# Kernel tuning notes

Hardware: AMD Instinct MI355X
Metric: run time of the kernel (lower is better)

Reference implementation:

```python
import jax, jax.numpy as jnp
import numpy as np

N_EMBD = 768
N_HEAD = 12
DIM_HEAD = N_EMBD // N_HEAD


def setup_inputs() -> dict:
    key = jax.random.key(0)
    k1, k2, k3 = jax.random.split(key, 3)
    B, T = 4, 2048
    x = jax.random.normal(k1, (B, T, N_EMBD), dtype=jnp.float32)
    # torch Linear(n_embd, 3*n_embd, bias=False): y = x @ W.T, W:[3C,C].
    # Store pre-transposed [C,3C] for direct matmul.
    s = 1.0 / np.sqrt(N_EMBD)
    W_qkv = jax.random.uniform(k2, (N_EMBD, 3 * N_EMBD), dtype=jnp.float32, minval=-s, maxval=s)
    W_proj = jax.random.uniform(k3, (N_EMBD, N_EMBD), dtype=jnp.float32, minval=-s, maxval=s)
    return {"x": x, "W_qkv": W_qkv, "W_proj": W_proj}


def reference(x, W_qkv, W_proj):
    B, T, C = x.shape
    qkv = x @ W_qkv                                  # [B,T,3C]
    q, k, v = jnp.split(qkv, 3, axis=-1)
    def heads(t):  # [B,T,C] -> [B,H,T,Dh]
        return t.reshape(B, T, N_HEAD, DIM_HEAD).transpose(0, 2, 1, 3)
    q, k, v = heads(q), heads(k), heads(v)
    # Source divides by scale = dim_head**-0.5, i.e. multiplies by sqrt(dim_head).
    scores = jnp.einsum('bhtd,bhsd->bhts', q, k) * jnp.sqrt(jnp.float32(DIM_HEAD))
    attn = jax.nn.softmax(scores, axis=-1)           # [B,H,T,T] materialized
    y = jnp.einsum('bhts,bhsd->bhtd', attn, v)       # [B,H,T,Dh]
    y = y.transpose(0, 2, 1, 3).reshape(B, T, C)
    return y @ W_proj
```

## Files before the change

kernel.cpp:

```cpp
#include <hip/hip_runtime.h>

typedef _Float16 f16;
typedef f16 f16x4 __attribute__((ext_vector_type(4)));
typedef f16 f16x8 __attribute__((ext_vector_type(8)));
typedef __fp16 h16x2 __attribute__((ext_vector_type(2)));
typedef float floatx4 __attribute__((ext_vector_type(4)));

#define LDT 72
#define LDE 136
#define QSCALE 11.5415603271117f

__device__ __forceinline__ void gld16(const void* g, void* l) {
  __builtin_amdgcn_global_load_lds((const __attribute__((address_space(1))) unsigned int*)g,
                                   (__attribute__((address_space(3))) unsigned int*)l,
                                   16, 0, 0);
}

__global__ __launch_bounds__(256) void cvt_f32_f16(const float* __restrict__ in,
                                                   f16* __restrict__ out) {
  size_t i = ((size_t)blockIdx.x * 256 + threadIdx.x) * 8;
  float4 v0 = *(const float4*)(in + i);
  float4 v1 = *(const float4*)(in + i + 4);
  f16x8 h = {(f16)v0.x, (f16)v0.y, (f16)v0.z, (f16)v0.w,
             (f16)v1.x, (f16)v1.y, (f16)v1.z, (f16)v1.w};
  *(f16x8*)(out + i) = h;
}

__global__ __launch_bounds__(256) void transpose_f32_f16_tiled(const float* __restrict__ in,
                                                               f16* __restrict__ out,
                                                               int K, int N) {
  __shared__ f16 tile[64][LDT];
  int k0 = blockIdx.x * 64, n0 = blockIdx.y * 64;
  int tid = threadIdx.x;
  int r = tid >> 4, c4 = (tid & 15) * 4;
  for (int p = 0; p < 4; ++p) {
    int rr = r + p * 16;
    float4 v = *(const float4*)(in + (size_t)(k0 + rr) * N + n0 + c4);
    tile[c4 + 0][rr] = (f16)v.x;
    tile[c4 + 1][rr] = (f16)v.y;
    tile[c4 + 2][rr] = (f16)v.z;
    tile[c4 + 3][rr] = (f16)v.w;
  }
  __syncthreads();
  int rn = tid >> 3, ck = (tid & 7) * 8;
  for (int p = 0; p < 2; ++p) {
    int rr = rn + p * 32;
    *(uint4*)(out + (size_t)(n0 + rr) * K + k0 + ck) = *(const uint4*)(&tile[rr][ck]);
  }
}

__global__ __launch_bounds__(256) void gemm1_qkv(const f16* __restrict__ A,
                                                 const f16* __restrict__ Bt,
                                                 f16* __restrict__ q16, f16* __restrict__ k16,
                                                 f16* __restrict__ vt) {
  __shared__ f16 smem[17408];
  f16* As = smem;
  f16* Bs = smem + 8192;
  int tid = threadIdx.x;
  int lane = tid & 63, wid = tid >> 6;
  int quad = lane >> 4, l16 = lane & 15;
  int wy = wid >> 1, wx = wid & 1;
  int m0 = blockIdx.x * 128, n0 = blockIdx.y * 128;
  int gr = lane >> 3, gc = (lane & 7) * 8;
  floatx4 acc[4][4] = {};
  for (int k0 = 0; k0 < 768; k0 += 64) {
    for (int p = 0; p < 4; ++p) {
      int c = wid * 4 + p;
      int row = c * 8 + gr;
      gld16(A + (size_t)(m0 + row) * 768 + k0 + gc, As + c * 512);
      gld16(Bt + (size_t)(n0 + row) * 768 + k0 + gc, Bs + c * 512);
    }
    __syncthreads();
    for (int kk = 0; kk < 64; kk += 32) {
      f16x8 af[4], bfr[4];
      for (int i = 0; i < 4; ++i)
        af[i] = *(const f16x8*)(As + (wy * 64 + i * 16 + l16) * 64 + kk + quad * 8);
      for (int j = 0; j < 4; ++j)
        bfr[j] = *(const f16x8*)(Bs + (wx * 64 + j * 16 + l16) * 64 + kk + quad * 8);
      for (int i = 0; i < 4; ++i)
        for (int j = 0; j < 4; ++j)
          acc[i][j] = __builtin_amdgcn_mfma_f32_16x16x32_f16(af[i], bfr[j], acc[i][j], 0, 0, 0);
    }
    __syncthreads();
  }
  int b = m0 >> 11, t0 = m0 & 2047;
  if (n0 < 1536) {
    for (int i = 0; i < 4; ++i)
      for (int j = 0; j < 4; ++j)
        for (int r = 0; r < 4; ++r) {
          int t = t0 + wy * 64 + i * 16 + quad * 4 + r;
          int col = n0 + wx * 64 + j * 16 + l16;
          float a = acc[i][j][r];
          if (col < 768) {
            int h = col >> 6, d = col & 63;
            q16[((size_t)(b * 12 + h)) * 131072 + (size_t)t * 64 + d] = (f16)(a * QSCALE);
          } else {
            int c = col - 768;
            int h = c >> 6, d = c & 63;
            k16[((size_t)(b * 12 + h)) * 131072 + (size_t)t * 64 + d] = (f16)a;
          }
        }
  } else {
    f16* Vtile = smem;
    int h0 = (n0 - 1536) >> 6;
    for (int i = 0; i < 4; ++i)
      for (int j = 0; j < 4; ++j) {
        int cl = wx * 64 + j * 16 + l16;
        int rl = wy * 64 + i * 16 + quad * 4;
        for (int r = 0; r < 4; ++r)
          Vtile[cl * LDE + rl + r] = (f16)acc[i][j][r];
      }
    __syncthreads();
    int u = tid & 15;
    for (int p = 0; p < 8; ++p) {
      int c = (tid >> 4) + p * 16;
      *(uint4*)(vt + ((size_t)(b * 12 + h0 + (c >> 6))) * 131072 +
                (size_t)(c & 63) * 2048 + t0 + u * 8) =
          *(const uint4*)(Vtile + c * LDE + u * 8);
    }
  }
}

__global__ __launch_bounds__(256) void gemm_bt_f16(const f16* __restrict__ A,
                                                   const f16* __restrict__ Bt,
                                                   float* __restrict__ C,
                                                   int M, int N, int K) {
  __shared__ f16 As[8192];
  __shared__ f16 Bs[8192];
  int tid = threadIdx.x;
  int lane = tid & 63, wid = tid >> 6;
  int quad = lane >> 4, l16 = lane & 15;
  int wy = wid >> 1, wx = wid & 1;
  int m0 = blockIdx.x * 128, n0 = blockIdx.y * 128;
  int gr = lane >> 3, gc = (lane & 7) * 8;
  floatx4 acc[4][4] = {};
  for (int k0 = 0; k0 < K; k0 += 64) {
    for (int p = 0; p < 4; ++p) {
      int c = wid * 4 + p;
      int row = c * 8 + gr;
      gld16(A + (size_t)(m0 + row) * K + k0 + gc, As + c * 512);
      gld16(Bt + (size_t)(n0 + row) * K + k0 + gc, Bs + c * 512);
    }
    __syncthreads();
    for (int kk = 0; kk < 64; kk += 32) {
      f16x8 af[4], bfr[4];
      for (int i = 0; i < 4; ++i)
        af[i] = *(const f16x8*)(As + (wy * 64 + i * 16 + l16) * 64 + kk + quad * 8);
      for (int j = 0; j < 4; ++j)
        bfr[j] = *(const f16x8*)(Bs + (wx * 64 + j * 16 + l16) * 64 + kk + quad * 8);
      for (int i = 0; i < 4; ++i)
        for (int j = 0; j < 4; ++j)
          acc[i][j] = __builtin_amdgcn_mfma_f32_16x16x32_f16(af[i], bfr[j], acc[i][j], 0, 0, 0);
    }
    __syncthreads();
  }
  for (int i = 0; i < 4; ++i) {
    int row = m0 + wy * 64 + i * 16 + quad * 4;
    for (int j = 0; j < 4; ++j) {
      int col = n0 + wx * 64 + j * 16 + l16;
      for (int r = 0; r < 4; ++r)
        C[(size_t)(row + r) * N + col] = acc[i][j][r];
    }
  }
}

__global__ __launch_bounds__(256, 1) void flash_attn(const f16* __restrict__ q16,
                                                     const f16* __restrict__ k16,
                                                     const f16* __restrict__ vT,
                                                     f16* __restrict__ y) {
  __shared__ f16 KsA[128 * 64];
  __shared__ f16 VtA[64 * 128];
  __shared__ f16 KsB[128 * 64];
  __shared__ f16 VtB[64 * 128];
  const int T = 2048;
  int xcd = blockIdx.x & 7, yb = blockIdx.x >> 3;
  int bh = xcd * 6 + (yb >> 4);
  int qt = yb & 15;
  int b = bh / 12, h = bh - b * 12;
  int tid = threadIdx.x;
  int lane = tid & 63, wid = tid >> 6;
  int quad = lane >> 4, l16 = lane & 15;
  size_t hb = (size_t)bh * T * 64;

  int kr = lane >> 3;
  int kcc = ((lane & 7) ^ kr) * 8;
  const f16* kbase = k16 + hb + (size_t)(wid * 32 + kr) * 64 + kcc;
  const f16* vbase0;
  const f16* vbase1;
  const f16* vbase2;
  const f16* vbase3;
  {
    int lr = lane >> 4, lc = lane & 15;
    vbase0 = vT + hb + (size_t)(wid * 16 + 0 + lr) * T + ((lc ^ (0 + lr)) * 8);
    vbase1 = vT + hb + (size_t)(wid * 16 + 4 + lr) * T + ((lc ^ (4 + lr)) * 8);
    vbase2 = vT + hb + (size_t)(wid * 16 + 8 + lr) * T + ((lc ^ (8 + lr)) * 8);
    vbase3 = vT + hb + (size_t)(wid * 16 + 12 + lr) * T + ((lc ^ (12 + lr)) * 8);
  }

#define STAGE(KD, VD, ktn)                                              \
  do {                                                                  \
    const f16* kp_ = kbase + (size_t)(ktn) * 8192;                      \
    gld16(kp_ + 0 * 512, (KD) + (wid * 4 + 0) * 512);                   \
    gld16(kp_ + 1 * 512, (KD) + (wid * 4 + 1) * 512);                   \
    gld16(kp_ + 2 * 512, (KD) + (wid * 4 + 2) * 512);                   \
    gld16(kp_ + 3 * 512, (KD) + (wid * 4 + 3) * 512);                   \
    gld16(vbase0 + (ktn) * 128, (VD) + (wid * 4 + 0) * 512);            \
    gld16(vbase1 + (ktn) * 128, (VD) + (wid * 4 + 1) * 512);            \
    gld16(vbase2 + (ktn) * 128, (VD) + (wid * 4 + 2) * 512);            \
    gld16(vbase3 + (ktn) * 128, (VD) + (wid * 4 + 3) * 512);            \
  } while (0)

  f16x8 qf[2][2];
#pragma unroll
  for (int g = 0; g < 2; ++g) {
    size_t qrow = hb + (size_t)(qt * 128 + wid * 32 + g * 16 + l16) * 64 + quad * 8;
    qf[g][0] = *(const f16x8*)(q16 + qrow);
    qf[g][1] = *(const f16x8*)(q16 + qrow + 32);
  }
  f16x4 ones4;
  for (int e = 0; e < 4; ++e) ones4[e] = (f16)1.0f;

  float m_i[2] = {-1e30f, -1e30f}, l_i[2] = {0.f, 0.f};
  floatx4 o[2][4] = {};

#define COMPUTE(KC, VC)                                                            \
  do {                                                                             \
    floatx4 sf[2][8] = {};                                                         \
    _Pragma("unroll") for (int kk = 0; kk < 2; ++kk)                               \
        _Pragma("unroll") for (int i = 0; i < 8; ++i) {                            \
      f16x8 kf = *(const f16x8*)((KC) + (i * 16 + l16) * 64 +                      \
                                 (((kk * 4 + quad) ^ (l16 & 7)) * 8));             \
      sf[0][i] = __builtin_amdgcn_mfma_f32_16x16x32_f16(kf, qf[0][kk], sf[0][i], 0, 0, 0); \
      sf[1][i] = __builtin_amdgcn_mfma_f32_16x16x32_f16(kf, qf[1][kk], sf[1][i], 0, 0, 0); \
    }                                                                              \
    f16x4 pf[2][8];                                                                \
    _Pragma("unroll") for (int g = 0; g < 2; ++g) {                                \
      float mx = fmaxf(fmaxf(sf[g][0][0], sf[g][0][1]), fmaxf(sf[g][0][2], sf[g][0][3])); \
      _Pragma("unroll") for (int i = 1; i < 8; ++i)                                \
          mx = fmaxf(mx, fmaxf(fmaxf(sf[g][i][0], sf[g][i][1]),                    \
                               fmaxf(sf[g][i][2], sf[g][i][3])));                  \
      mx = fmaxf(mx, __shfl_xor(mx, 16));                                          \
      mx = fmaxf(mx, __shfl_xor(mx, 32));                                          \
      float m_new = fmaxf(m_i[g], mx);                                             \
      float alpha = exp2f(m_i[g] - m_new);                                         \
      m_i[g] = m_new;                                                              \
      _Pragma("unroll") for (int i = 0; i < 4; ++i) o[g][i] *= alpha;              \
      _Pragma("unroll") for (int i = 0; i < 8; ++i) {                              \
        union { h16x2 hh; f16 ff[2]; } a2, b2;                                     \
        a2.hh = __builtin_amdgcn_cvt_pkrtz(sf[g][i][0] - m_new, sf[g][i][1] - m_new); \
        b2.hh = __builtin_amdgcn_cvt_pkrtz(sf[g][i][2] - m_new, sf[g][i][3] - m_new); \
        f16x4 uu = {a2.ff[0], a2.ff[1], b2.ff[0], b2.ff[1]};                       \
        pf[g][i] = __builtin_elementwise_exp2(uu);                                 \
      }                                                                            \
      floatx4 rs = {0.f, 0.f, 0.f, 0.f};                                           \
      _Pragma("unroll") for (int si = 0; si < 8; ++si)                             \
          rs = __builtin_amdgcn_mfma_f32_16x16x16f16(ones4, pf[g][si], rs, 0, 0, 0); \
      l_i[g] = l_i[g] * alpha + rs[0];                                             \
    }                                                                              \
    _Pragma("unroll") for (int i = 0; i < 4; ++i)                                  \
        _Pragma("unroll") for (int si = 0; si < 8; ++si) {                         \
      int cch = si * 2 + (quad >> 1);                                              \
      f16x4 vf = *(const f16x4*)((VC) + (i * 16 + l16) * 128 + ((cch ^ l16) * 8) + \
                                 (quad & 1) * 4);                                  \
      o[0][i] = __builtin_amdgcn_mfma_f32_16x16x16f16(vf, pf[0][si], o[0][i], 0, 0, 0); \
      o[1][i] = __builtin_amdgcn_mfma_f32_16x16x16f16(vf, pf[1][si], o[1][i], 0, 0, 0); \
    }                                                                              \
  } while (0)

  STAGE(KsA, VtA, 0);
  __syncthreads();

#pragma unroll 1
  for (int kt2 = 0; kt2 < 8; ++kt2) {
    STAGE(KsB, VtB, 2 * kt2 + 1);
    COMPUTE(KsA, VtA);
    __syncthreads();
    if (kt2 < 7) STAGE(KsA, VtA, 2 * kt2 + 2);
    COMPUTE(KsB, VtB);
    if (kt2 < 7) __syncthreads();
  }

#pragma unroll
  for (int g = 0; g < 2; ++g) {
    float invl = 1.0f / l_i[g];
    int t = qt * 128 + wid * 32 + g * 16 + l16;
    size_t off = ((size_t)(b * T + t)) * 768 + h * 64;
    for (int i = 0; i < 4; ++i)
      for (int r = 0; r < 4; ++r)
        y[off + i * 16 + quad * 4 + r] = (f16)(o[g][i][r] * invl);
  }
#undef STAGE
#undef COMPUTE
}

extern "C" void kernel_launch(void* const* d_in, const int* in_sizes, int n_in,
                              void* d_out, int out_size, void* d_ws, size_t ws_size,
                              hipStream_t stream) {
  const float* x     = (const float*)d_in[0];
  const float* Wqkv  = (const float*)d_in[1];
  const float* Wproj = (const float*)d_in[2];
  float* out = (float*)d_out;
  char* ws = (char*)d_ws;
  f16* q16    = (f16*)ws;
  f16* k16    = (f16*)(ws + 12582912);
  f16* vT16   = (f16*)(ws + 25165824);
  f16* y16    = (f16*)(ws + 37748736);
  f16* WqkvT  = (f16*)(ws + 50331648);
  f16* WprojT = (f16*)(ws + 53870592);
  f16* x16 = y16;

  cvt_f32_f16<<<3072, 256, 0, stream>>>(x, x16);
  transpose_f32_f16_tiled<<<dim3(12, 36), 256, 0, stream>>>(Wqkv, WqkvT, 768, 2304);
  transpose_f32_f16_tiled<<<dim3(12, 12), 256, 0, stream>>>(Wproj, WprojT, 768, 768);
  gemm1_qkv<<<dim3(64, 18), 256, 0, stream>>>(x16, WqkvT, q16, k16, vT16);
  flash_attn<<<768, 256, 0, stream>>>(q16, k16, vT16, y16);
  gemm_bt_f16<<<dim3(64, 6), 256, 0, stream>>>(y16, WprojT, out, 8192, 768, 768);
}
```

Measured before the change: 253.4 us.

## Add lazy softmax rescaling, MFMA priority hints and precomputed LDS addressing in flash attention

```diff
diff --git a/kernel.cpp b/kernel.cpp
--- a/kernel.cpp
+++ b/kernel.cpp
@@ -168,10 +168,7 @@
                                                      const f16* __restrict__ k16,
                                                      const f16* __restrict__ vT,
                                                      f16* __restrict__ y) {
-  __shared__ f16 KsA[128 * 64];
-  __shared__ f16 VtA[64 * 128];
-  __shared__ f16 KsB[128 * 64];
-  __shared__ f16 VtB[64 * 128];
+  __shared__ f16 lds[32768];
   const int T = 2048;
   int xcd = blockIdx.x & 7, yb = blockIdx.x >> 3;
   int bh = xcd * 6 + (yb >> 4);
@@ -197,17 +194,25 @@
     vbase3 = vT + hb + (size_t)(wid * 16 + 12 + lr) * T + ((lc ^ (12 + lr)) * 8);
   }
 
-#define STAGE(KD, VD, ktn)                                              \
+  const f16* pK[2];
+  pK[0] = lds + l16 * 64 + ((quad ^ (l16 & 7)) * 8);
+  pK[1] = lds + l16 * 64 + (((4 + quad) ^ (l16 & 7)) * 8);
+  const f16* pV[8];
+#pragma unroll
+  for (int si = 0; si < 8; ++si)
+    pV[si] = lds + l16 * 128 + (((si * 2 + (quad >> 1)) ^ l16) * 8) + (quad & 1) * 4;
+
+#define STAGE(KOFF, VOFF, ktn)                                          \
   do {                                                                  \
     const f16* kp_ = kbase + (size_t)(ktn) * 8192;                      \
-    gld16(kp_ + 0 * 512, (KD) + (wid * 4 + 0) * 512);                   \
-    gld16(kp_ + 1 * 512, (KD) + (wid * 4 + 1) * 512);                   \
-    gld16(kp_ + 2 * 512, (KD) + (wid * 4 + 2) * 512);                   \
-    gld16(kp_ + 3 * 512, (KD) + (wid * 4 + 3) * 512);                   \
-    gld16(vbase0 + (ktn) * 128, (VD) + (wid * 4 + 0) * 512);            \
-    gld16(vbase1 + (ktn) * 128, (VD) + (wid * 4 + 1) * 512);            \
-    gld16(vbase2 + (ktn) * 128, (VD) + (wid * 4 + 2) * 512);            \
-    gld16(vbase3 + (ktn) * 128, (VD) + (wid * 4 + 3) * 512);            \
+    gld16(kp_ + 0 * 512, lds + (KOFF) + (wid * 4 + 0) * 512);           \
+    gld16(kp_ + 1 * 512, lds + (KOFF) + (wid * 4 + 1) * 512);           \
+    gld16(kp_ + 2 * 512, lds + (KOFF) + (wid * 4 + 2) * 512);           \
+    gld16(kp_ + 3 * 512, lds + (KOFF) + (wid * 4 + 3) * 512);           \
+    gld16(vbase0 + (ktn) * 128, lds + (VOFF) + (wid * 4 + 0) * 512);    \
+    gld16(vbase1 + (ktn) * 128, lds + (VOFF) + (wid * 4 + 1) * 512);    \
+    gld16(vbase2 + (ktn) * 128, lds + (VOFF) + (wid * 4 + 2) * 512);    \
+    gld16(vbase3 + (ktn) * 128, lds + (VOFF) + (wid * 4 + 3) * 512);    \
   } while (0)
 
   f16x8 qf[2][2];
@@ -219,64 +224,87 @@
   }
   f16x4 ones4;
   for (int e = 0; e < 4; ++e) ones4[e] = (f16)1.0f;
+  const floatx4 Z4 = {0.f, 0.f, 0.f, 0.f};
 
   float m_i[2] = {-1e30f, -1e30f}, l_i[2] = {0.f, 0.f};
   floatx4 o[2][4] = {};
 
-#define COMPUTE(KC, VC)                                                            \
+#define COMPUTE(KOFF, VOFF)                                                        \
   do {                                                                             \
-    floatx4 sf[2][8] = {};                                                         \
-    _Pragma("unroll") for (int kk = 0; kk < 2; ++kk)                               \
-        _Pragma("unroll") for (int i = 0; i < 8; ++i) {                            \
-      f16x8 kf = *(const f16x8*)((KC) + (i * 16 + l16) * 64 +                      \
-                                 (((kk * 4 + quad) ^ (l16 & 7)) * 8));             \
-      sf[0][i] = __builtin_amdgcn_mfma_f32_16x16x32_f16(kf, qf[0][kk], sf[0][i], 0, 0, 0); \
-      sf[1][i] = __builtin_amdgcn_mfma_f32_16x16x32_f16(kf, qf[1][kk], sf[1][i], 0, 0, 0); \
-    }                                                                              \
+    floatx4 sf[2][8];                                                              \
+    __builtin_amdgcn_s_setprio(1);                                                 \
+    _Pragma("unroll") for (int i = 0; i < 8; ++i) {                                \
+      f16x8 kf = *(const f16x8*)(pK[0] + (KOFF) + i * 1024);                       \
+      sf[0][i] = __builtin_amdgcn_mfma_f32_16x16x32_f16(kf, qf[0][0], Z4, 0, 0, 0); \
+      sf[1][i] = __builtin_amdgcn_mfma_f32_16x16x32_f16(kf, qf[1][0], Z4, 0, 0, 0); \
+    }                                                                              \
+    _Pragma("unroll") for (int i = 0; i < 8; ++i) {                                \
+      f16x8 kf = *(const f16x8*)(pK[1] + (KOFF) + i * 1024);                       \
+      sf[0][i] = __builtin_amdgcn_mfma_f32_16x16x32_f16(kf, qf[0][1], sf[0][i], 0, 0, 0); \
+      sf[1][i] = __builtin_amdgcn_mfma_f32_16x16x32_f16(kf, qf[1][1], sf[1][i], 0, 0, 0); \
+    }                                                                              \
+    __builtin_amdgcn_s_setprio(0);                                                 \
     f16x4 pf[2][8];                                                                \
     _Pragma("unroll") for (int g = 0; g < 2; ++g) {                                \
-      float mx = fmaxf(fmaxf(sf[g][0][0], sf[g][0][1]), fmaxf(sf[g][0][2], sf[g][0][3])); \
-      _Pragma("unroll") for (int i = 1; i < 8; ++i)                                \
-          mx = fmaxf(mx, fmaxf(fmaxf(sf[g][i][0], sf[g][i][1]),                    \
-                               fmaxf(sf[g][i][2], sf[g][i][3])));                  \
+      float t0_ = fmaxf(fmaxf(sf[g][0][0], sf[g][0][1]), fmaxf(sf[g][0][2], sf[g][0][3])); \
+      float t1_ = fmaxf(fmaxf(sf[g][1][0], sf[g][1][1]), fmaxf(sf[g][1][2], sf[g][1][3])); \
+      float t2_ = fmaxf(fmaxf(sf[g][2][0], sf[g][2][1]), fmaxf(sf[g][2][2], sf[g][2][3])); \
+      float t3_ = fmaxf(fmaxf(sf[g][3][0], sf[g][3][1]), fmaxf(sf[g][3][2], sf[g][3][3])); \
+      float t4_ = fmaxf(fmaxf(sf[g][4][0], sf[g][4][1]), fmaxf(sf[g][4][2], sf[g][4][3])); \
+      float t5_ = fmaxf(fmaxf(sf[g][5][0], sf[g][5][1]), fmaxf(sf[g][5][2], sf[g][5][3])); \
+      float t6_ = fmaxf(fmaxf(sf[g][6][0], sf[g][6][1]), fmaxf(sf[g][6][2], sf[g][6][3])); \
+      float t7_ = fmaxf(fmaxf(sf[g][7][0], sf[g][7][1]), fmaxf(sf[g][7][2], sf[g][7][3])); \
+      float mx = fmaxf(fmaxf(fmaxf(t0_, t1_), fmaxf(t2_, t3_)),                    \
+                       fmaxf(fmaxf(t4_, t5_), fmaxf(t6_, t7_)));                   \
       mx = fmaxf(mx, __shfl_xor(mx, 16));                                          \
       mx = fmaxf(mx, __shfl_xor(mx, 32));                                          \
-      float m_new = fmaxf(m_i[g], mx);                                             \
-      float alpha = exp2f(m_i[g] - m_new);                                         \
-      m_i[g] = m_new;                                                              \
-      _Pragma("unroll") for (int i = 0; i < 4; ++i) o[g][i] *= alpha;              \
+      if (__any(mx > m_i[g] + 8.0f)) {                                             \
+        float m_new = fmaxf(m_i[g], mx);                                           \
+        float alpha = exp2f(m_i[g] - m_new);                                       \
+        m_i[g] = m_new;                                                            \
+        _Pragma("unroll") for (int i = 0; i < 4; ++i) o[g][i] *= alpha;            \
+        l_i[g] *= alpha;                                                           \
+      }                                                                            \
+      float mi_ = m_i[g];                                                          \
       _Pragma("unroll") for (int i = 0; i < 8; ++i) {                              \
         union { h16x2 hh; f16 ff[2]; } a2, b2;                                     \
-        a2.hh = __builtin_amdgcn_cvt_pkrtz(sf[g][i][0] - m_new, sf[g][i][1] - m_new); \
-        b2.hh = __builtin_amdgcn_cvt_pkrtz(sf[g][i][2] - m_new, sf[g][i][3] - m_new); \
+        a2.hh = __builtin_amdgcn_cvt_pkrtz(sf[g][i][0] - mi_, sf[g][i][1] - mi_);  \
+        b2.hh = __builtin_amdgcn_cvt_pkrtz(sf[g][i][2] - mi_, sf[g][i][3] - mi_);  \
         f16x4 uu = {a2.ff[0], a2.ff[1], b2.ff[0], b2.ff[1]};                       \
         pf[g][i] = __builtin_elementwise_exp2(uu);                                 \
       }                                                                            \
-      floatx4 rs = {0.f, 0.f, 0.f, 0.f};                                           \
-      _Pragma("unroll") for (int si = 0; si < 8; ++si)                             \
-          rs = __builtin_amdgcn_mfma_f32_16x16x16f16(ones4, pf[g][si], rs, 0, 0, 0); \
-      l_i[g] = l_i[g] * alpha + rs[0];                                             \
+    }                                                                              \
+    __builtin_amdgcn_s_setprio(1);                                                 \
+    _Pragma("unroll") for (int g = 0; g < 2; ++g) {                                \
+      floatx4 rs0 = __builtin_amdgcn_mfma_f32_16x16x16f16(ones4, pf[g][0], Z4, 0, 0, 0); \
+      floatx4 rs1 = __builtin_amdgcn_mfma_f32_16x16x16f16(ones4, pf[g][4], Z4, 0, 0, 0); \
+      rs0 = __builtin_amdgcn_mfma_f32_16x16x16f16(ones4, pf[g][1], rs0, 0, 0, 0);  \
+      rs1 = __builtin_amdgcn_mfma_f32_16x16x16f16(ones4, pf[g][5], rs1, 0, 0, 0);  \
+      rs0 = __builtin_amdgcn_mfma_f32_16x16x16f16(ones4, pf[g][2], rs0, 0, 0, 0);  \
+      rs1 = __builtin_amdgcn_mfma_f32_16x16x16f16(ones4, pf[g][6], rs1, 0, 0, 0);  \
+      rs0 = __builtin_amdgcn_mfma_f32_16x16x16f16(ones4, pf[g][3], rs0, 0, 0, 0);  \
+      rs1 = __builtin_amdgcn_mfma_f32_16x16x16f16(ones4, pf[g][7], rs1, 0, 0, 0);  \
+      l_i[g] += rs0[0] + rs1[0];                                                   \
     }                                                                              \
     _Pragma("unroll") for (int i = 0; i < 4; ++i)                                  \
         _Pragma("unroll") for (int si = 0; si < 8; ++si) {                         \
-      int cch = si * 2 + (quad >> 1);                                              \
-      f16x4 vf = *(const f16x4*)((VC) + (i * 16 + l16) * 128 + ((cch ^ l16) * 8) + \
-                                 (quad & 1) * 4);                                  \
+      f16x4 vf = *(const f16x4*)(pV[si] + (VOFF) + i * 2048);                      \
       o[0][i] = __builtin_amdgcn_mfma_f32_16x16x16f16(vf, pf[0][si], o[0][i], 0, 0, 0); \
       o[1][i] = __builtin_amdgcn_mfma_f32_16x16x16f16(vf, pf[1][si], o[1][i], 0, 0, 0); \
     }                                                                              \
+    __builtin_amdgcn_s_setprio(0);                                                 \
   } while (0)
 
-  STAGE(KsA, VtA, 0);
+  STAGE(0, 16384, 0);
   __syncthreads();
 
 #pragma unroll 1
   for (int kt2 = 0; kt2 < 8; ++kt2) {
-    STAGE(KsB, VtB, 2 * kt2 + 1);
-    COMPUTE(KsA, VtA);
-    __syncthreads();
-    if (kt2 < 7) STAGE(KsA, VtA, 2 * kt2 + 2);
-    COMPUTE(KsB, VtB);
+    STAGE(8192, 24576, 2 * kt2 + 1);
+    COMPUTE(0, 16384);
+    __syncthreads();
+    if (kt2 < 7) STAGE(0, 16384, 2 * kt2 + 2);
+    COMPUTE(8192, 24576);
     if (kt2 < 7) __syncthreads();
   }
 
```

Result: slower. 291.8 us (+15.2%).
